# Performance work log

Measured on AMD Instinct MI355X. Metric: run time of the kernel, lower is better.

## Reference

```python
import jax, jax.numpy as jnp
import numpy as np

N_USERS = 100000
N_ITEMS = 500000
DIM = 64
N_SCORE = 256


def setup_inputs() -> dict:
    key = jax.random.key(0)
    k1, k2, k3 = jax.random.split(key, 3)
    score_user_ids = jax.random.randint(k1, (N_SCORE,), 0, N_USERS)
    user_embeddings = jax.random.normal(k2, (N_USERS, DIM), dtype=jnp.float32)
    item_embeddings = jax.random.normal(k3, (N_ITEMS, DIM), dtype=jnp.float32)
    return {
        "score_user_ids": score_user_ids,
        "user_embeddings": user_embeddings,
        "item_embeddings": item_embeddings,
    }


def reference(score_user_ids, user_embeddings, item_embeddings):
    # CML._create_score_items: scores[u, i] = -sum_d (U[u,d] - I[i,d])^2
    # Expressed via the ||u||^2 + ||i||^2 - 2 u.i decomposition (same math,
    # avoids materializing the [U, I, D] broadcast intermediate).
    u = user_embeddings[score_user_ids]                 # [U, D]
    u_sq = jnp.sum(u * u, axis=1, keepdims=True)        # [U, 1]
    i_sq = jnp.sum(item_embeddings * item_embeddings, axis=1)  # [I]
    cross = jnp.einsum('ud,id->ui', u, item_embeddings)        # [U, I]
    scores = -(u_sq + i_sq[None, :] - 2.0 * cross)      # [U, I]
    return scores
```

## Files before the change

### kernel.cpp

```cpp
#include <hip/hip_runtime.h>
#include <hip/hip_bf16.h>


#define DIM 64
#define NSCORE 256

typedef short bf16x8 __attribute__((ext_vector_type(8)));
typedef float f32x4 __attribute__((ext_vector_type(4)));

__device__ __forceinline__ short f2bf(float f) {
    union { float f; unsigned u; } v; v.f = f;
    unsigned r = v.u + 0x7FFF + ((v.u >> 16) & 1);
    return (short)(r >> 16);
}

__global__ void prep_users(const int* __restrict__ uid,
                           const float* __restrict__ U,
                           short* __restrict__ wsA,
                           float* __restrict__ ws_usq) {
    int t = blockIdx.x * blockDim.x + threadIdx.x;
    int u   = t >> 4;
    int seg = t & 15;
    int id = uid[u];
    float4 x = *(const float4*)(U + (long)id * DIM + seg * 4);
    float s = x.x * x.x + x.y * x.y + x.z * x.z + x.w * x.w;
    #pragma unroll
    for (int off = 1; off < 16; off <<= 1) s += __shfl_xor(s, off, 16);
    if (seg == 0) ws_usq[u] = s;

    int ks   = seg >> 3;
    int quad = (seg & 7) >> 1;
    int j0   = (seg & 1) * 4;
    int ut   = u >> 4;
    int lane = quad * 16 + (u & 15);
    short4 b;
    b.x = f2bf(x.x); b.y = f2bf(x.y); b.z = f2bf(x.z); b.w = f2bf(x.w);
    *(short4*)(wsA + (ut * 2 + ks) * 512 + lane * 8 + j0) = b;
}

#define BROW 72

__global__ __launch_bounds__(256)
void cml_main(const float* __restrict__ I,
              const short* __restrict__ wsA,
              const float* __restrict__ ws_usq,
              float* __restrict__ out,
              int n_items) {
    __shared__ __align__(16) short sB[64 * BROW];
    __shared__ float sIsq[64];
    __shared__ float sUsq[NSCORE];

    int t  = threadIdx.x;
    int i0 = blockIdx.x * 64;

    sUsq[t] = ws_usq[t];

    #pragma unroll
    for (int c = 0; c < 4; c++) {
        int f   = c * 256 + t;
        int row = f >> 4;
        int seg = f & 15;
        int gi  = i0 + row;
        float4 x = make_float4(0.f, 0.f, 0.f, 0.f);
        if (gi < n_items)
            x = *(const float4*)(I + (long)gi * DIM + seg * 4);
        float s = x.x * x.x + x.y * x.y + x.z * x.z + x.w * x.w;
        #pragma unroll
        for (int off = 1; off < 16; off <<= 1) s += __shfl_xor(s, off, 16);
        short4 b;
        b.x = f2bf(x.x); b.y = f2bf(x.y); b.z = f2bf(x.z); b.w = f2bf(x.w);
        *(short4*)(sB + row * BROW + seg * 4) = b;
        if (seg == 0) sIsq[row] = s;
    }
    __syncthreads();

    int w    = t >> 6;
    int l    = t & 63;
    int m16  = l & 15;
    int quad = l >> 4;

    const short* bp = sB + (16 * w + m16) * BROW + quad * 8;
    bf16x8 bfr0 = *(const bf16x8*)(bp);
    bf16x8 bfr1 = *(const bf16x8*)(bp + 32);

    f32x4 acc[16];
    #pragma unroll
    for (int ut = 0; ut < 16; ut++) acc[ut] = (f32x4){0.f, 0.f, 0.f, 0.f};

    const bf16x8* Afrag = (const bf16x8*)wsA;
    #pragma unroll
    for (int ut = 0; ut < 16; ut++) {
        bf16x8 a0 = Afrag[(ut * 2 + 0) * 64 + l];
        bf16x8 a1 = Afrag[(ut * 2 + 1) * 64 + l];
        acc[ut] = __builtin_amdgcn_mfma_f32_16x16x32_bf16(a0, bfr0, acc[ut], 0, 0, 0);
        acc[ut] = __builtin_amdgcn_mfma_f32_16x16x32_bf16(a1, bfr1, acc[ut], 0, 0, 0);
    }

    int nloc = 16 * w + m16;
    int gi   = i0 + nloc;
    if (gi < n_items) {
        float isq = sIsq[nloc];
        #pragma unroll
        for (int ut = 0; ut < 16; ut++) {
            int u0 = ut * 16 + quad * 4;
            #pragma unroll
            for (int r = 0; r < 4; r++) {
                int u = u0 + r;
                out[(size_t)u * n_items + gi] = 2.0f * acc[ut][r] - sUsq[u] - isq;
            }
        }
    }
}

extern "C" void kernel_launch(void* const* d_in, const int* in_sizes, int n_in,
                              void* d_out, int out_size, void* d_ws, size_t ws_size,
                              hipStream_t stream) {
    const int*   uid = (const int*)d_in[0];
    const float* U   = (const float*)d_in[1];
    const float* I   = (const float*)d_in[2];
    float*       out = (float*)d_out;
    int n_items = in_sizes[2] / DIM;

    short* wsA    = (short*)d_ws;
    float* ws_usq = (float*)((char*)d_ws + (size_t)NSCORE * DIM * sizeof(short));

    prep_users<<<16, 256, 0, stream>>>(uid, U, wsA, ws_usq);
    int nblocks = (n_items + 63) / 64;
    cml_main<<<nblocks, 256, 0, stream>>>(I, wsA, ws_usq, out, n_items);
}
```

Before: 643.0 us.

## Split users across blocks and load item fragments directly into registers

Restructures the main kernel so each block handles 64 users by 256 items, with each wave loading item rows directly into MFMA B fragments instead of staging them through shared memory. The item squared-norm reduction uses cross-lane shuffles, and per-user norms and A fragments are held in registers. This removes the shared-memory staging and barrier and cuts accumulator registers to raise occupancy. In exchange, item embeddings are re-read once per user group.

```diff
diff --git a/kernel.cpp b/kernel.cpp
--- a/kernel.cpp
+++ b/kernel.cpp
@@ -38,75 +38,79 @@
     *(short4*)(wsA + (ut * 2 + ks) * 512 + lane * 8 + j0) = b;
 }
 
-#define BROW 72
-
 __global__ __launch_bounds__(256)
 void cml_main(const float* __restrict__ I,
               const short* __restrict__ wsA,
               const float* __restrict__ ws_usq,
               float* __restrict__ out,
               int n_items) {
-    __shared__ __align__(16) short sB[64 * BROW];
-    __shared__ float sIsq[64];
-    __shared__ float sUsq[NSCORE];
-
     int t  = threadIdx.x;
-    int i0 = blockIdx.x * 64;
-
-    sUsq[t] = ws_usq[t];
-
-    #pragma unroll
-    for (int c = 0; c < 4; c++) {
-        int f   = c * 256 + t;
-        int row = f >> 4;
-        int seg = f & 15;
-        int gi  = i0 + row;
-        float4 x = make_float4(0.f, 0.f, 0.f, 0.f);
-        if (gi < n_items)
-            x = *(const float4*)(I + (long)gi * DIM + seg * 4);
-        float s = x.x * x.x + x.y * x.y + x.z * x.z + x.w * x.w;
-        #pragma unroll
-        for (int off = 1; off < 16; off <<= 1) s += __shfl_xor(s, off, 16);
-        short4 b;
-        b.x = f2bf(x.x); b.y = f2bf(x.y); b.z = f2bf(x.z); b.w = f2bf(x.w);
-        *(short4*)(sB + row * BROW + seg * 4) = b;
-        if (seg == 0) sIsq[row] = s;
-    }
-    __syncthreads();
+    int ug = blockIdx.x & 3;
+    int ig = blockIdx.x >> 2;
+    int i0 = ig * 256;
 
     int w    = t >> 6;
     int l    = t & 63;
     int m16  = l & 15;
     int quad = l >> 4;
 
-    const short* bp = sB + (16 * w + m16) * BROW + quad * 8;
-    bf16x8 bfr0 = *(const bf16x8*)(bp);
-    bf16x8 bfr1 = *(const bf16x8*)(bp + 32);
+    bf16x8 a[4][2];
+    const bf16x8* Af = (const bf16x8*)wsA;
+    #pragma unroll
+    for (int ut = 0; ut < 4; ut++)
+        #pragma unroll
+        for (int ks = 0; ks < 2; ks++)
+            a[ut][ks] = Af[((ug * 4 + ut) * 2 + ks) * 64 + l];
 
-    f32x4 acc[16];
+    float us[4][4];
     #pragma unroll
-    for (int ut = 0; ut < 16; ut++) acc[ut] = (f32x4){0.f, 0.f, 0.f, 0.f};
+    for (int ut = 0; ut < 4; ut++)
+        #pragma unroll
+        for (int r = 0; r < 4; r++)
+            us[ut][r] = ws_usq[ug * 64 + ut * 16 + quad * 4 + r];
 
-    const bf16x8* Afrag = (const bf16x8*)wsA;
+    size_t row0 = (size_t)(ug * 64 + quad * 4) * n_items;
+
     #pragma unroll
-    for (int ut = 0; ut < 16; ut++) {
-        bf16x8 a0 = Afrag[(ut * 2 + 0) * 64 + l];
-        bf16x8 a1 = Afrag[(ut * 2 + 1) * 64 + l];
-        acc[ut] = __builtin_amdgcn_mfma_f32_16x16x32_bf16(a0, bfr0, acc[ut], 0, 0, 0);
-        acc[ut] = __builtin_amdgcn_mfma_f32_16x16x32_bf16(a1, bfr1, acc[ut], 0, 0, 0);
-    }
+    for (int it = 0; it < 4; it++) {
+        int gi = i0 + w * 64 + it * 16 + m16;
+        const float* rp = I + (size_t)gi * DIM + quad * 8;
+        float4 x0 = make_float4(0.f,0.f,0.f,0.f), x1 = x0, x2 = x0, x3 = x0;
+        if (gi < n_items) {
+            x0 = *(const float4*)(rp);
+            x1 = *(const float4*)(rp + 4);
+            x2 = *(const float4*)(rp + 32);
+            x3 = *(const float4*)(rp + 36);
+        }
+        float s = x0.x*x0.x + x0.y*x0.y + x0.z*x0.z + x0.w*x0.w
+                + x1.x*x1.x + x1.y*x1.y + x1.z*x1.z + x1.w*x1.w
+                + x2.x*x2.x + x2.y*x2.y + x2.z*x2.z + x2.w*x2.w
+                + x3.x*x3.x + x3.y*x3.y + x3.z*x3.z + x3.w*x3.w;
+        s += __shfl_xor(s, 16);
+        s += __shfl_xor(s, 32);
 
-    int nloc = 16 * w + m16;
-    int gi   = i0 + nloc;
-    if (gi < n_items) {
-        float isq = sIsq[nloc];
+        bf16x8 b0, b1;
+        b0[0]=f2bf(x0.x); b0[1]=f2bf(x0.y); b0[2]=f2bf(x0.z); b0[3]=f2bf(x0.w);
+        b0[4]=f2bf(x1.x); b0[5]=f2bf(x1.y); b0[6]=f2bf(x1.z); b0[7]=f2bf(x1.w);
+        b1[0]=f2bf(x2.x); b1[1]=f2bf(x2.y); b1[2]=f2bf(x2.z); b1[3]=f2bf(x2.w);
+        b1[4]=f2bf(x3.x); b1[5]=f2bf(x3.y); b1[6]=f2bf(x3.z); b1[7]=f2bf(x3.w);
+
+        f32x4 acc[4];
         #pragma unroll
-        for (int ut = 0; ut < 16; ut++) {
-            int u0 = ut * 16 + quad * 4;
+        for (int ut = 0; ut < 4; ut++) {
+            acc[ut] = (f32x4){0.f, 0.f, 0.f, 0.f};
+            acc[ut] = __builtin_amdgcn_mfma_f32_16x16x32_bf16(a[ut][0], b0, acc[ut], 0, 0, 0);
+            acc[ut] = __builtin_amdgcn_mfma_f32_16x16x32_bf16(a[ut][1], b1, acc[ut], 0, 0, 0);
+        }
+
+        if (gi < n_items) {
             #pragma unroll
-            for (int r = 0; r < 4; r++) {
-                int u = u0 + r;
-                out[(size_t)u * n_items + gi] = 2.0f * acc[ut][r] - sUsq[u] - isq;
+            for (int ut = 0; ut < 4; ut++) {
+                #pragma unroll
+                for (int r = 0; r < 4; r++) {
+                    out[row0 + (size_t)(ut * 16 + r) * n_items + gi] =
+                        2.0f * acc[ut][r] - us[ut][r] - s;
+                }
             }
         }
     }
@@ -125,6 +129,6 @@
     float* ws_usq = (float*)((char*)d_ws + (size_t)NSCORE * DIM * sizeof(short));
 
     prep_users<<<16, 256, 0, stream>>>(uid, U, wsA, ws_usq);
-    int nblocks = (n_items + 63) / 64;
-    cml_main<<<nblocks, 256, 0, stream>>>(I, wsA, ws_usq, out, n_items);
+    int nig = (n_items + 255) / 256;
+    cml_main<<<nig * 4, 256, 0, stream>>>(I, wsA, ws_usq, out, n_items);
 }
```

Measured after the change: 748.4 us. +16.4%, slower.
